# Optimization experiments

Hardware: AMD Instinct MI355X
Metric: run time of the kernel (lower is better)

The kernel has to match this reference:

```python
import jax, jax.numpy as jnp
import numpy as np
import math

MU = 50.0
NBIT = 6


def _make_quant_tables(nbit):
    # Faithful to the torch __init__: basis=[1/(2^n-1)*2^i], level_code = binary
    # code of i  =>  levels[i] = i / (2^nbit - 1) (already sorted ascending).
    num_levels = 2 ** nbit
    levels = np.arange(num_levels, dtype=np.float32) / np.float32(num_levels - 1)
    # thrs_mul @ levels = midpoints of adjacent levels, shape (num_levels-1,)
    thrs = 0.5 * (levels[:-1] + levels[1:])
    return jnp.asarray(levels), jnp.asarray(thrs)


def setup_inputs() -> dict:
    key = jax.random.key(0)
    # sigmoid-like codeword values in [0, 1]
    x = jax.random.uniform(key, (65536, 512), dtype=jnp.float32)
    levels, thrs = _make_quant_tables(NBIT)
    return {"x": x, "thrs": thrs, "levels": levels}


def reference(x, thrs, levels):
    log1mu = math.log(1.0 + MU)
    xr = x
    # ---- compress (mu-law) ----
    xm = 2.0 * x - 1.0                      # [B, D] in [-1, 1]
    x_sign = jnp.where(xm > 0, 1.0, -1.0)
    xc = jnp.log1p(MU * jnp.abs(xm)) / log1mu
    # ---- quantize: y = levels[#(thrs < xc)] (collapses 63 sequential where's) ----
    idx = jnp.searchsorted(thrs, xc, side="left")  # count of thrs strictly < xc
    y = levels[idx]
    # ---- decompress ----
    yd = (jnp.exp(y * log1mu) - 1.0) / MU
    yd = yd * x_sign
    yd = (yd + 1.0) / 2.0
    # ---- SNR norm ----
    snr = jnp.mean(jnp.linalg.norm(xr, axis=1) / jnp.linalg.norm(xr - yd, axis=1))
    return yd, snr
```

## Files before the change

kernel.cpp:

```cpp
#include <hip/hip_runtime.h>
#include <hip/hip_bf16.h>
#include <math.h>


#define NROWS 65536
#define DCOL  512
#define ROWS_PER_BLOCK 4
#define NBLOCKS (NROWS / ROWS_PER_BLOCK)

#define K_IDX  11.1063604f
#define K_EXP  0.0624099307f

__device__ __forceinline__ float process_one(float xi, float& sx, float& se) {
    float xm = fmaf(2.0f, xi, -1.0f);
    float s  = (xm > 0.0f) ? 0.5f : -0.5f;
    float a  = fabsf(xm);
    float w  = fmaf(50.0f, a, 1.0f);
    float qf = floorf(fmaf(__log2f(w), K_IDX, 0.5f));
    float e2 = __expf(qf * K_EXP);
    float da = fmaf(e2, 0.02f, -0.02f);
    float out = fmaf(s, da, 0.5f);
    sx = fmaf(xi, xi, sx);
    float e = xi - out;
    se = fmaf(e, e, se);
    return out;
}

__global__ __launch_bounds__(256) void quant_main(const float* __restrict__ x,
                                                  float* __restrict__ yd,
                                                  float* __restrict__ partial) {
    const int wave = threadIdx.x >> 6;
    const int lane = threadIdx.x & 63;
    const int row  = blockIdx.x * ROWS_PER_BLOCK + wave;

    const float4* __restrict__ xr = (const float4*)(x  + (size_t)row * DCOL);
    float4*       __restrict__ yr = (float4*)      (yd + (size_t)row * DCOL);

    float sx = 0.0f, se = 0.0f;

#pragma unroll
    for (int h = 0; h < 2; ++h) {
        float4 v = xr[h * 64 + lane];
        float4 o;
        o.x = process_one(v.x, sx, se);
        o.y = process_one(v.y, sx, se);
        o.z = process_one(v.z, sx, se);
        o.w = process_one(v.w, sx, se);
        yr[h * 64 + lane] = o;
    }

#pragma unroll
    for (int off = 32; off >= 1; off >>= 1) {
        sx += __shfl_xor(sx, off);
        se += __shfl_xor(se, off);
    }

    __shared__ float ls[ROWS_PER_BLOCK];
    if (lane == 0) {
        ls[wave] = sqrtf(sx / se) * (1.0f / (float)NROWS);
    }
    __syncthreads();
    if (threadIdx.x == 0) {
        partial[blockIdx.x] = ls[0] + ls[1] + ls[2] + ls[3];
    }
}

__global__ __launch_bounds__(256) void snr_reduce(const float* __restrict__ partial,
                                                  float* __restrict__ snr_out) {
    __shared__ float s[256];
    float acc = 0.0f;
    for (int i = threadIdx.x; i < NBLOCKS; i += 256) acc += partial[i];
    s[threadIdx.x] = acc;
    __syncthreads();
#pragma unroll
    for (int off = 128; off >= 1; off >>= 1) {
        if (threadIdx.x < off) s[threadIdx.x] += s[threadIdx.x + off];
        __syncthreads();
    }
    if (threadIdx.x == 0) snr_out[0] = s[0];
}

extern "C" void kernel_launch(void* const* d_in, const int* in_sizes, int n_in,
                              void* d_out, int out_size, void* d_ws, size_t ws_size,
                              hipStream_t stream) {
    const float* x = (const float*)d_in[0];
    float* yd      = (float*)d_out;
    float* snr_out = (float*)d_out + (size_t)NROWS * DCOL;
    float* partial = (float*)d_ws;

    quant_main<<<NBLOCKS, 256, 0, stream>>>(x, yd, partial);
    snr_reduce<<<1, 256, 0, stream>>>(partial, snr_out);
}
```

Before: 249.6 us.

## Process four rows per wave with batched loads and nontemporal stores

Each wave now handles four rows instead of one. All eight float4 loads are issued up front so more memory requests are in flight per wave, and the grid shrinks by four times. Output stores use nontemporal hints to avoid polluting cache, and the sign application is simplified with copysign. The cost is higher register pressure and fewer blocks to hide latency across CUs.

```diff
diff --git a/kernel.cpp b/kernel.cpp
--- a/kernel.cpp
+++ b/kernel.cpp
@@ -5,25 +5,31 @@
 
 #define NROWS 65536
 #define DCOL  512
-#define ROWS_PER_BLOCK 4
+#define ROWS_PER_WAVE 4
+#define WAVES_PER_BLOCK 4
+#define ROWS_PER_BLOCK (ROWS_PER_WAVE * WAVES_PER_BLOCK)
 #define NBLOCKS (NROWS / ROWS_PER_BLOCK)
 
 #define K_IDX  11.1063604f
 #define K_EXP  0.0624099307f
 
-__device__ __forceinline__ float process_one(float xi, float& sx, float& se) {
-    float xm = fmaf(2.0f, xi, -1.0f);
-    float s  = (xm > 0.0f) ? 0.5f : -0.5f;
-    float a  = fabsf(xm);
-    float w  = fmaf(50.0f, a, 1.0f);
-    float qf = floorf(fmaf(__log2f(w), K_IDX, 0.5f));
-    float e2 = __expf(qf * K_EXP);
-    float da = fmaf(e2, 0.02f, -0.02f);
-    float out = fmaf(s, da, 0.5f);
-    sx = fmaf(xi, xi, sx);
-    float e = xi - out;
-    se = fmaf(e, e, se);
-    return out;
+typedef float vfloat4 __attribute__((ext_vector_type(4)));
+
+__device__ __forceinline__ void process4(vfloat4 v, vfloat4& o, float& sx, float& se) {
+#pragma unroll
+    for (int k = 0; k < 4; ++k) {
+        float xi = v[k];
+        float xm = fmaf(2.0f, xi, -1.0f);
+        float w  = fmaf(50.0f, fabsf(xm), 1.0f);
+        float qf = floorf(fmaf(__log2f(w), K_IDX, 0.5f));
+        float e2 = __expf(qf * K_EXP);
+        float da = fmaf(e2, 0.01f, -0.01f);
+        float out = 0.5f + copysignf(da, xm);
+        sx = fmaf(xi, xi, sx);
+        float e = xi - out;
+        se = fmaf(e, e, se);
+        o[k] = out;
+    }
 }
 
 __global__ __launch_bounds__(256) void quant_main(const float* __restrict__ x,
@@ -31,34 +37,50 @@
                                                   float* __restrict__ partial) {
     const int wave = threadIdx.x >> 6;
     const int lane = threadIdx.x & 63;
-    const int row  = blockIdx.x * ROWS_PER_BLOCK + wave;
+    const int row0 = (blockIdx.x * WAVES_PER_BLOCK + wave) * ROWS_PER_WAVE;
 
-    const float4* __restrict__ xr = (const float4*)(x  + (size_t)row * DCOL);
-    float4*       __restrict__ yr = (float4*)      (yd + (size_t)row * DCOL);
+    const vfloat4* __restrict__ xr[ROWS_PER_WAVE];
+    vfloat4*       __restrict__ yr[ROWS_PER_WAVE];
+#pragma unroll
+    for (int r = 0; r < ROWS_PER_WAVE; ++r) {
+        xr[r] = (const vfloat4*)(x  + (size_t)(row0 + r) * DCOL);
+        yr[r] = (vfloat4*)      (yd + (size_t)(row0 + r) * DCOL);
+    }
 
-    float sx = 0.0f, se = 0.0f;
+    vfloat4 va[ROWS_PER_WAVE], vb[ROWS_PER_WAVE];
+#pragma unroll
+    for (int r = 0; r < ROWS_PER_WAVE; ++r) {
+        va[r] = xr[r][lane];
+        vb[r] = xr[r][64 + lane];
+    }
+
+    float sx[ROWS_PER_WAVE], se[ROWS_PER_WAVE];
+#pragma unroll
+    for (int r = 0; r < ROWS_PER_WAVE; ++r) { sx[r] = 0.0f; se[r] = 0.0f; }
 
 #pragma unroll
-    for (int h = 0; h < 2; ++h) {
-        float4 v = xr[h * 64 + lane];
-        float4 o;
-        o.x = process_one(v.x, sx, se);
-        o.y = process_one(v.y, sx, se);
-        o.z = process_one(v.z, sx, se);
-        o.w = process_one(v.w, sx, se);
-        yr[h * 64 + lane] = o;
+    for (int r = 0; r < ROWS_PER_WAVE; ++r) {
+        vfloat4 oa, ob;
+        process4(va[r], oa, sx[r], se[r]);
+        process4(vb[r], ob, sx[r], se[r]);
+        __builtin_nontemporal_store(oa, &yr[r][lane]);
+        __builtin_nontemporal_store(ob, &yr[r][64 + lane]);
     }
 
+    float acc = 0.0f;
 #pragma unroll
-    for (int off = 32; off >= 1; off >>= 1) {
-        sx += __shfl_xor(sx, off);
-        se += __shfl_xor(se, off);
+    for (int r = 0; r < ROWS_PER_WAVE; ++r) {
+        float s1 = sx[r], s2 = se[r];
+#pragma unroll
+        for (int off = 32; off >= 1; off >>= 1) {
+            s1 += __shfl_xor(s1, off);
+            s2 += __shfl_xor(s2, off);
+        }
+        acc += sqrtf(s1 / s2);
     }
 
-    __shared__ float ls[ROWS_PER_BLOCK];
-    if (lane == 0) {
-        ls[wave] = sqrtf(sx / se) * (1.0f / (float)NROWS);
-    }
+    __shared__ float ls[WAVES_PER_BLOCK];
+    if (lane == 0) ls[wave] = acc * (1.0f / (float)NROWS);
     __syncthreads();
     if (threadIdx.x == 0) {
         partial[blockIdx.x] = ls[0] + ls[1] + ls[2] + ls[3];
```

Result: faster. 241.7 us (-3.1%).
